# Kernel optimization log

Measured on AMD Instinct MI355X. Metric: run time of the kernel, lower is better.

Reference implementation:

```python
import jax, jax.numpy as jnp
import numpy as np
from jax.scipy.special import logsumexp

PAD_IDX, SOS_IDX, EOS_IDX = 0, 1, 2
NEG = -10000.0


def setup_inputs() -> dict:
    B, T, L = 64, 256, 8
    K, E, H = 128, 256, 512      # num_tags, EMBED_SIZE, HIDDEN_SIZE
    CV, WV = 128, 50000          # char / word vocab
    key = jax.random.key(0)
    ks = jax.random.split(key, 12)
    lengths = jax.random.randint(ks[0], (B,), T // 2, T + 1)
    mask = jnp.arange(T)[None, :] < lengths[:, None]          # [B,T] contiguous prefix
    wx = jnp.where(mask, jax.random.randint(ks[1], (B, T), 3, WV), 0).astype(jnp.int32)
    cx = jax.random.randint(ks[2], (B, T, L), 0, CV).astype(jnp.int32)
    y_body = jnp.where(mask, jax.random.randint(ks[3], (B, T), 3, K), PAD_IDX)
    y = jnp.concatenate([jnp.full((B, 1), SOS_IDX, jnp.int32), y_body.astype(jnp.int32)], 1)  # [B,T+1]
    s = 0.05
    char_emb = s * jax.random.normal(ks[4], (CV, E), jnp.float32)
    word_emb = s * jax.random.normal(ks[5], (WV, E), jnp.float32)
    Wi = s * jax.random.normal(ks[6], (E, 4 * H), jnp.float32)
    Wh = s * jax.random.normal(ks[7], (H, 4 * H), jnp.float32)
    b = jnp.zeros((4 * H,), jnp.float32)
    Wout = s * jax.random.normal(ks[8], (H, K), jnp.float32)
    bout = jnp.zeros((K,), jnp.float32)
    trans = jax.random.normal(ks[9], (K, K), jnp.float32)
    trans = trans.at[SOS_IDX, :].set(NEG)
    trans = trans.at[:, EOS_IDX].set(NEG)
    trans = trans.at[:, PAD_IDX].set(NEG)
    trans = trans.at[PAD_IDX, :].set(NEG)
    trans = trans.at[PAD_IDX, EOS_IDX].set(0.0)
    trans = trans.at[PAD_IDX, PAD_IDX].set(0.0)
    return dict(cx=cx, wx=wx, y=y, char_emb=char_emb, word_emb=word_emb,
                Wi=Wi, Wh=Wh, b=b, Wout=Wout, bout=bout, trans=trans)


def _forward(cx, wx, y, char_emb, word_emb, Wi, Wh, b, Wout, bout, trans):
    B, T = wx.shape
    K = trans.shape[0]
    H = Wh.shape[0]
    mask = (wx > 0)                                            # [B,T] bool
    maskf = mask.astype(jnp.float32)
    # embedding: word lookup + mean-pooled char lookup
    x = word_emb[wx] + char_emb[cx].mean(axis=2)               # [B,T,E]

    # masked LSTM (equivalent to pack_padded for prefix masks)
    def lstm_step(carry, inp):
        h, c = carry
        xt, mt = inp                                            # [B,E], [B,1]
        z = xt @ Wi + h @ Wh + b                                # [B,4H]
        i, f, g, o = jnp.split(z, 4, axis=-1)
        i, f, o = jax.nn.sigmoid(i), jax.nn.sigmoid(f), jax.nn.sigmoid(o)
        c_new = f * c + i * jnp.tanh(g)
        h_new = o * jnp.tanh(c_new)
        h = jnp.where(mt, h_new, h)
        c = jnp.where(mt, c_new, c)
        return (h, c), h

    h0 = jnp.zeros((B, H), x.dtype)
    xs = jnp.swapaxes(x, 0, 1)                                  # [T,B,E]
    ms = jnp.swapaxes(mask, 0, 1)[..., None]                    # [T,B,1]
    _, hs = jax.lax.scan(lstm_step, (h0, h0), (xs, ms))         # [T,B,H]
    hs = jnp.swapaxes(hs, 0, 1)                                 # [B,T,H]
    h = (hs @ Wout + bout) * maskf[..., None]                   # emissions [B,T,K]

    # CRF forward algorithm (log partition Z)
    score0 = jnp.full((B, K), NEG, h.dtype).at[:, SOS_IDX].set(0.0)

    def crf_step(score, inp):
        em, mt = inp                                            # [B,K], [B,1]
        s_t = logsumexp(score[:, None, :] + em[:, :, None] + trans[None, :, :], axis=-1)
        return jnp.where(mt, s_t, score), None

    emT = jnp.swapaxes(h, 0, 1)                                 # [T,B,K]
    scoreZ, _ = jax.lax.scan(crf_step, score0, (emT, ms))
    Z = logsumexp(scoreZ + trans[EOS_IDX], axis=-1)             # [B]

    # gold path score
    y_prev, y_next = y[:, :-1], y[:, 1:]                        # [B,T]
    emit = jnp.take_along_axis(h, y_next[..., None], axis=-1)[..., 0]  # [B,T]
    tr = trans[y_next, y_prev]                                  # [B,T]
    gold = jnp.sum((emit + tr) * maskf, axis=1)                 # [B]
    lengths = mask.sum(axis=1)
    last_tag = y[jnp.arange(B), lengths]                        # y has T+1 cols
    gold = gold + trans[EOS_IDX, last_tag]
    return Z - gold                                             # NLL per sequence [B]


def reference(cx, wx, y, char_emb, word_emb, Wi, Wh, b, Wout, bout, trans):
    return _forward(cx, wx, y, char_emb, word_emb, Wi, Wh, b, Wout, bout, trans)
```

## Files before the change

kernel.cpp:

```cpp
#include <hip/hip_runtime.h>


typedef float f32x4 __attribute__((ext_vector_type(4)));
typedef float f32x16 __attribute__((ext_vector_type(16)));
typedef __bf16 bf16x8 __attribute__((ext_vector_type(8)));
typedef unsigned int u32x4 __attribute__((ext_vector_type(4)));
typedef unsigned int u32x2 __attribute__((ext_vector_type(2)));

#define T_LEN 256
#define BB    64
#define EE    256
#define HH    512
#define KK    128
#define KCAT  768

static __device__ inline unsigned f2bf(float f) {
  union { float f; unsigned u; } v; v.f = f;
  unsigned r = v.u + 0x7FFF + ((v.u >> 16) & 1);
  return r >> 16;
}
static __device__ inline float sigm(float x) { return 1.f / (1.f + __expf(-x)); }
static __device__ inline float tanh_fast(float x) {
  return 1.f - 2.f / (1.f + __expf(2.f * x));
}
static __device__ inline bf16x8 ubf(u32x4 v) {
  union { u32x4 u; bf16x8 b; } c; c.u = v; return c.b;
}

__global__ __launch_bounds__(256) void build_wcat(
    const float* __restrict__ Wi, const float* __restrict__ Wh,
    unsigned short* __restrict__ WcatT) {
  __shared__ float tile[64][65];
  int ct = blockIdx.x & 31, kt = blockIdx.x >> 5;
  int tc = threadIdx.x & 63, tr = threadIdx.x >> 6;
  int c0 = ct * 64, k0 = kt * 64;
#pragma unroll
  for (int i = 0; i < 16; ++i) {
    int r = tr * 16 + i, k = k0 + r;
    float v = (k < EE) ? Wi[(size_t)k * 2048 + c0 + tc]
                       : Wh[(size_t)(k - EE) * 2048 + c0 + tc];
    tile[r][tc] = v;
  }
  __syncthreads();
#pragma unroll
  for (int i = 0; i < 16; ++i) {
    int cL = tr * 16 + i;
    WcatT[(size_t)(c0 + cL) * KCAT + k0 + tc] = (unsigned short)f2bf(tile[tc][cL]);
  }
}

__global__ __launch_bounds__(256) void build_wout(
    const float* __restrict__ Wout, unsigned short* __restrict__ WoutT) {
  __shared__ float tile[64][65];
  int ct = blockIdx.x & 1, kt = blockIdx.x >> 1;
  int tc = threadIdx.x & 63, tr = threadIdx.x >> 6;
  int c0 = ct * 64, k0 = kt * 64;
#pragma unroll
  for (int i = 0; i < 16; ++i) {
    int r = tr * 16 + i;
    tile[r][tc] = Wout[(size_t)(k0 + r) * KK + c0 + tc];
  }
  __syncthreads();
#pragma unroll
  for (int i = 0; i < 16; ++i) {
    int cL = tr * 16 + i;
    WoutT[(size_t)(c0 + cL) * HH + k0 + tc] = (unsigned short)f2bf(tile[tc][cL]);
  }
}

__global__ __launch_bounds__(256) void embed_kernel(
    const int* __restrict__ wx, const int* __restrict__ cx,
    const float* __restrict__ we, const float* __restrict__ ce,
    unsigned short* __restrict__ x) {
  int bid = blockIdx.x;
  int t = bid >> 6, b = bid & 63;
  int e = threadIdx.x;
  int w = wx[b * T_LEN + t];
  float v = we[(size_t)w * EE + e];
  const int* cp = cx + ((size_t)(b * T_LEN + t)) * 8;
  float s = 0.f;
#pragma unroll
  for (int l = 0; l < 8; ++l) s += ce[(size_t)cp[l] * EE + e];
  v += s * 0.125f;
  x[(size_t)bid * EE + e] = (unsigned short)f2bf(v);
}

__global__ void zero_flags(unsigned int* __restrict__ f) {
  int i = threadIdx.x;
  if (i < 320) {
    unsigned z = 0u;
    asm volatile("global_store_dword %0, %1, off sc1"
                 :: "v"(f + i), "v"(z) : "memory");
  }
}

#define SBAR __builtin_amdgcn_sched_barrier(0)
#define WAITV(N) do { asm volatile("s_waitcnt vmcnt(" #N ")" ::: "memory"); SBAR; } while (0)
#define LDN(dst, ptr, OFF) \
  asm volatile("global_load_dwordx4 %0, %1, off offset:" OFF \
               : "=v"(dst) : "v"(ptr) : "memory")

#define ISSUE_X(B, P) do { \
  LDN(B[0],P,"0");   LDN(B[1],P,"32");  LDN(B[2],P,"64");  LDN(B[3],P,"96"); \
  LDN(B[4],P,"128"); LDN(B[5],P,"160"); LDN(B[6],P,"192"); LDN(B[7],P,"224"); \
  LDN(B[8],P,"256"); LDN(B[9],P,"288"); LDN(B[10],P,"320"); LDN(B[11],P,"352"); \
  LDN(B[12],P,"384"); LDN(B[13],P,"416"); LDN(B[14],P,"448"); LDN(B[15],P,"480"); } while (0)
#define ISSUE_H1(B, P) do { \
  LDN(B[0],P,"512"); LDN(B[1],P,"544"); LDN(B[2],P,"576"); LDN(B[3],P,"608"); \
  LDN(B[4],P,"640"); LDN(B[5],P,"672"); LDN(B[6],P,"704"); LDN(B[7],P,"736"); \
  LDN(B[8],P,"768"); LDN(B[9],P,"800"); LDN(B[10],P,"832"); LDN(B[11],P,"864"); \
  LDN(B[12],P,"896"); LDN(B[13],P,"928"); LDN(B[14],P,"960"); LDN(B[15],P,"992"); } while (0)

#define GATES_STORE(T) do { \
    bool mk = ((int)wxv) > 0; \
    _Pragma("unroll") \
    for (int r = 0; r < 4; ++r) { \
      float zi = acc[r], zf = acc[4 + r], zg = acc[8 + r], zo = acc[12 + r]; \
      float cn = sigm(zf) * cst[r] + sigm(zi) * tanh_fast(zg); \
      float hn = sigm(zo) * tanh_fast(cn); \
      if (mk) { cst[r] = cn; hst[r] = hn; } \
    } \
    u32x2 ph; \
    ph[0] = f2bf(hst[0]) | (f2bf(hst[1]) << 16); \
    ph[1] = f2bf(hst[2]) | (f2bf(hst[3]) << 16); \
    asm volatile("global_store_dwordx2 %0, %1, off sc1" \
                 :: "v"(hstore + (size_t)(T) * 65536), "v"(ph) : "memory"); \
  } while (0)

__global__ __launch_bounds__(128, 1) void fused_kernel(
    const unsigned short* __restrict__ x,
    unsigned short* __restrict__ hs,
    const unsigned short* __restrict__ WcatT,
    const unsigned short* __restrict__ WoutT,
    const float* __restrict__ bias,
    const float* __restrict__ bout,
    const float* __restrict__ trans,
    const int* __restrict__ wx,
    const int* __restrict__ y,
    float* __restrict__ em,
    unsigned int* __restrict__ flags,
    unsigned int* __restrict__ emflag,
    float* __restrict__ out) {
  __shared__ float s_tl[KK][129];
  __shared__ float s_El[KK][129];
  __shared__ float s_p[KK];
  __shared__ float s_red[16];

  const int bid = blockIdx.x;
  const int tid = threadIdx.x;
  const int wave = tid >> 6, lane = tid & 63;

  if (bid < 64) {
    const int bhalf = wave;
    const int hi = lane >> 5;
    const int batch = bhalf * 32 + (lane & 31);
    const int u0 = bid * 8;
    const int rr = lane & 31;
    const int wcol = (rr >> 3) * HH + u0 + (rr & 7);

    bf16x8 wreg[48];
#pragma unroll
    for (int kf = 0; kf < 48; ++kf)
      wreg[kf] = *(const bf16x8*)(WcatT + (size_t)wcol * KCAT + kf * 16 + hi * 8);

    float bv[16];
#pragma unroll
    for (int q = 0; q < 4; ++q)
#pragma unroll
      for (int r = 0; r < 4; ++r)
        bv[q * 4 + r] = bias[q * HH + u0 + 4 * hi + r];

    const char* xlane  = (const char*)x  + ((size_t)batch * EE + hi * 8) * 2;
    const char* hread  = (const char*)hs + ((size_t)batch * HH + hi * 8) * 2;
    char*       hstore = (char*)hs + ((size_t)batch * HH + u0 + 4 * hi) * 2;
    const int*  wxp    = wx + batch * T_LEN;

    float cst[4] = {0.f, 0.f, 0.f, 0.f};
    float hst[4] = {0.f, 0.f, 0.f, 0.f};
    u32x4 bufX[16], bufH[16];
    unsigned wxv;
    f32x16 acc;

    ISSUE_X(bufX, xlane);
    asm volatile("global_load_dword %0, %1, off" : "=v"(wxv) : "v"(wxp) : "memory");
    WAITV(0);
#pragma unroll
    for (int i = 0; i < 16; ++i) acc[i] = bv[i];
#pragma unroll
    for (int kf = 0; kf < 16; ++kf)
      acc = __builtin_amdgcn_mfma_f32_32x32x16_bf16(wreg[kf], ubf(bufX[kf]), acc, 0, 0, 0);
    GATES_STORE(0);
    WAITV(0);
    __syncthreads();
    if (tid == 0)
      __hip_atomic_store(flags + bid, 1u, __ATOMIC_RELAXED, __HIP_MEMORY_SCOPE_AGENT);

    for (int t = 1; t < T_LEN; ++t) {
      const char* xt = xlane + (size_t)t * 32768;
      const char* hp = hread + (size_t)(t - 1) * 65536;

      ISSUE_X(bufX, xt);
      asm volatile("global_load_dword %0, %1, off" : "=v"(wxv) : "v"(wxp + t) : "memory");
      {
        unsigned v;
        do {
          asm volatile("global_load_dword %0, %1, off sc1\n\ts_waitcnt vmcnt(0)"
                       : "=v"(v) : "v"(flags + lane) : "memory");
        } while (!__all((int)(v >= (unsigned)t)));
        SBAR;
      }
      ISSUE_X(bufH, hp);
#pragma unroll
      for (int i = 0; i < 16; ++i) acc[i] = bv[i];
#pragma unroll
      for (int kf = 0; kf < 16; ++kf)
        acc = __builtin_amdgcn_mfma_f32_32x32x16_bf16(wreg[kf], ubf(bufX[kf]), acc, 0, 0, 0);
      SBAR;
      ISSUE_H1(bufX, hp);
      WAITV(16);
#pragma unroll
      for (int kf = 0; kf < 16; ++kf)
        acc = __builtin_amdgcn_mfma_f32_32x32x16_bf16(wreg[16 + kf], ubf(bufH[kf]), acc, 0, 0, 0);
      WAITV(0);
#pragma unroll
      for (int kf = 0; kf < 16; ++kf)
        acc = __builtin_amdgcn_mfma_f32_32x32x16_bf16(wreg[32 + kf], ubf(bufX[kf]), acc, 0, 0, 0);
      GATES_STORE(t);
      WAITV(0);
      __syncthreads();
      if (tid == 0)
        __hip_atomic_store(flags + bid, (unsigned)(t + 1),
                           __ATOMIC_RELAXED, __HIP_MEMORY_SCOPE_AGENT);
    }
  } else if (bid < 72) {
    const int et0 = bid - 64;
    const int arow = lane & 15, kg4 = (lane >> 4) * 8;
    for (int i = 0; i < 32; ++i) {
      const int t = et0 + 8 * i;
      {
        unsigned v; int it = 0;
        for (;;) {
          asm volatile("global_load_dword %0, %1, off sc1\n\ts_waitcnt vmcnt(0)"
                       : "=v"(v) : "v"(flags + lane) : "memory");
          if (__all((int)(v >= (unsigned)(t + 1)))) break;
          if (++it >= (1 << 17)) break;
        }
        SBAR;
      }
      const unsigned short* A0 = hs + ((size_t)t * BB + wave * 32 + arow) * HH + kg4;
      f32x4 acc2[2][8];
#pragma unroll
      for (int mt = 0; mt < 2; ++mt)
#pragma unroll
        for (int nt = 0; nt < 8; ++nt) acc2[mt][nt] = (f32x4){0.f, 0.f, 0.f, 0.f};
#pragma unroll
      for (int ks = 0; ks < 16; ++ks) {
        bf16x8 a0 = *(const bf16x8*)(A0 + ks * 32);
        bf16x8 a1 = *(const bf16x8*)(A0 + 16 * HH + ks * 32);
#pragma unroll
        for (int nt = 0; nt < 8; ++nt) {
          bf16x8 bf = *(const bf16x8*)(WoutT + (size_t)(nt * 16 + arow) * HH + kg4 + ks * 32);
          acc2[0][nt] = __builtin_amdgcn_mfma_f32_16x16x32_bf16(a0, bf, acc2[0][nt], 0, 0, 0);
          acc2[1][nt] = __builtin_amdgcn_mfma_f32_16x16x32_bf16(a1, bf, acc2[1][nt], 0, 0, 0);
        }
      }
#pragma unroll
      for (int nt = 0; nt < 8; ++nt) {
        int n = nt * 16 + arow;
        float bo = bout[n];
#pragma unroll
        for (int mt = 0; mt < 2; ++mt)
#pragma unroll
          for (int r = 0; r < 4; ++r) {
            int row = t * BB + wave * 32 + mt * 16 + (lane >> 4) * 4 + r;
            float val = acc2[mt][nt][r] + bo;
            asm volatile("global_store_dword %0, %1, off sc1"
                         :: "v"(em + (size_t)row * KK + n), "v"(val) : "memory");
          }
      }
      WAITV(0);
      __syncthreads();
      if (tid == 0)
        __hip_atomic_store(emflag + t, 1u, __ATOMIC_RELAXED, __HIP_MEMORY_SCOPE_AGENT);
    }
  } else {
    const int b = bid - 72;
    const int k = tid;
    for (int i2 = tid; i2 < KK * KK; i2 += 128) {
      float v = trans[i2];
      s_tl[i2 >> 7][i2 & 127] = v;
      s_El[i2 >> 7][i2 & 127] = __expf(v);
    }
    __syncthreads();
    float sck = (k == 1) ? 0.f : -10000.f;
    float msc = 0.f;

    for (int t = 0; t < T_LEN; ++t) {
      if (wx[b * T_LEN + t] <= 0) continue;
      {
        unsigned v; int it = 0;
        for (;;) {
          asm volatile("global_load_dword %0, %1, off sc1\n\ts_waitcnt vmcnt(0)"
                       : "=v"(v) : "v"(emflag + t) : "memory");
          if (v) break;
          if (++it >= (1 << 17)) break;
        }
        SBAR;
      }
      s_p[k] = __expf(sck - msc);
      __syncthreads();
      float S = 0.f;
#pragma unroll
      for (int j = 0; j < KK; ++j) S += s_El[k][j] * s_p[j];
      float ns = em[((size_t)t * BB + b) * KK + k] + msc + __logf(S);
      sck = ns;
      float m = ns;
#pragma unroll
      for (int off = 32; off; off >>= 1) m = fmaxf(m, __shfl_xor(m, off));
      if (lane == 0) s_red[8 + wave] = m;
      __syncthreads();
      msc = fmaxf(s_red[8], s_red[9]);
    }

    float term = 0.f, cnt = 0.f;
#pragma unroll
    for (int rep = 0; rep < 2; ++rep) {
      int tt = tid + rep * 128;
      int yp = y[b * 257 + tt], yn = y[b * 257 + tt + 1];
      if (wx[b * T_LEN + tt] > 0) {
        term += em[((size_t)tt * BB + b) * KK + yn] + s_tl[yn][yp];
        cnt += 1.f;
      }
    }
#pragma unroll
    for (int off = 32; off; off >>= 1) {
      term += __shfl_xor(term, off);
      cnt += __shfl_xor(cnt, off);
    }
    if (lane == 0) { s_red[wave] = term; s_red[2 + wave] = cnt; }
    __syncthreads();
    float gold = s_red[0] + s_red[1];
    int len = (int)(s_red[2] + s_red[3] + 0.5f);

    float v = sck + s_tl[2][k];
    float mz = v;
#pragma unroll
    for (int off = 32; off; off >>= 1) mz = fmaxf(mz, __shfl_xor(mz, off));
    if (lane == 0) s_red[4 + wave] = mz;
    __syncthreads();
    mz = fmaxf(s_red[4], s_red[5]);
    float e = __expf(v - mz);
#pragma unroll
    for (int off = 32; off; off >>= 1) e += __shfl_xor(e, off);
    if (lane == 0) s_red[6 + wave] = e;
    __syncthreads();
    if (tid == 0) {
      float Z = mz + __logf(s_red[6] + s_red[7]);
      int last_tag = y[b * 257 + len];
      out[b] = Z - (gold + s_tl[2][last_tag]);
    }
  }
}

extern "C" void kernel_launch(void* const* d_in, const int* in_sizes, int n_in,
                              void* d_out, int out_size, void* d_ws, size_t ws_size,
                              hipStream_t stream) {
  const int*   cx    = (const int*)d_in[0];
  const int*   wx    = (const int*)d_in[1];
  const int*   y     = (const int*)d_in[2];
  const float* ce    = (const float*)d_in[3];
  const float* we    = (const float*)d_in[4];
  const float* Wi    = (const float*)d_in[5];
  const float* Wh    = (const float*)d_in[6];
  const float* bias  = (const float*)d_in[7];
  const float* Wout  = (const float*)d_in[8];
  const float* bout  = (const float*)d_in[9];
  const float* trans = (const float*)d_in[10];
  float* out = (float*)d_out;

  char* ws = (char*)d_ws;
  unsigned short* WcatT = (unsigned short*)(ws + 0);
  unsigned short* WoutT = (unsigned short*)(ws + 3145728);
  unsigned short* x     = (unsigned short*)(ws + 3276800);
  unsigned short* hs    = (unsigned short*)(ws + 11665408);
  unsigned int*   flags = (unsigned int*)(ws + 28442624);
  unsigned int*   emflag= (unsigned int*)(ws + 28442880);
  float*          em    = (float*)(ws + 28444672);

  build_wcat<<<384, 256, 0, stream>>>(Wi, Wh, WcatT);
  build_wout<<<16, 256, 0, stream>>>(Wout, WoutT);
  embed_kernel<<<T_LEN * BB, 256, 0, stream>>>(wx, cx, we, ce, x);
  zero_flags<<<1, 320, 0, stream>>>(flags);
  fused_kernel<<<136, 128, 0, stream>>>(x, hs, WcatT, WoutT, bias, bout, trans,
                                        wx, y, em, flags, emflag, out);
}
```

Measured before the change: 1.463 ms.

## Split LSTM into per-batch-group blocks with local flags and fuse emission into CRF

Restructures the persistent LSTM kernel so 128 blocks each handle 8 batch rows and a 32-unit slice using 16x16 MFMAs. Each block now waits only on the 16 producer blocks of its own batch group, through a ring of non-coherent flags with a fallback to coherent polling, instead of on all 64 blocks. The separate emission-projection blocks and the em buffer are removed: each CRF block computes its emissions and gold score from the hidden state with a dot product per timestep. The intent is to cut global synchronisation latency per step and drop the extra em stage. The cost is more CRF work per step and relaxed-visibility flag reads.

```diff
diff --git a/kernel.cpp b/kernel.cpp
--- a/kernel.cpp
+++ b/kernel.cpp
@@ -2,10 +2,8 @@
 
 
 typedef float f32x4 __attribute__((ext_vector_type(4)));
-typedef float f32x16 __attribute__((ext_vector_type(16)));
 typedef __bf16 bf16x8 __attribute__((ext_vector_type(8)));
 typedef unsigned int u32x4 __attribute__((ext_vector_type(4)));
-typedef unsigned int u32x2 __attribute__((ext_vector_type(2)));
 
 #define T_LEN 256
 #define BB    64
@@ -18,6 +16,10 @@
   union { float f; unsigned u; } v; v.f = f;
   unsigned r = v.u + 0x7FFF + ((v.u >> 16) & 1);
   return r >> 16;
+}
+static __device__ inline float bf2f(unsigned short u) {
+  union { unsigned u; float f; } v; v.u = ((unsigned)u) << 16;
+  return v.f;
 }
 static __device__ inline float sigm(float x) { return 1.f / (1.f + __expf(-x)); }
 static __device__ inline float tanh_fast(float x) {
@@ -86,8 +88,8 @@
 }
 
 __global__ void zero_flags(unsigned int* __restrict__ f) {
-  int i = threadIdx.x;
-  if (i < 320) {
+  int i = blockIdx.x * 256 + threadIdx.x;
+  if (i < 128 + 64 * 128) {
     unsigned z = 0u;
     asm volatile("global_store_dword %0, %1, off sc1"
                  :: "v"(f + i), "v"(z) : "memory");
@@ -95,39 +97,21 @@
 }
 
 #define SBAR __builtin_amdgcn_sched_barrier(0)
-#define WAITV(N) do { asm volatile("s_waitcnt vmcnt(" #N ")" ::: "memory"); SBAR; } while (0)
-#define LDN(dst, ptr, OFF) \
+#define WAIT0 do { asm volatile("s_waitcnt vmcnt(0)" ::: "memory"); SBAR; } while (0)
+#define LDN(dst, p, OFF) \
   asm volatile("global_load_dwordx4 %0, %1, off offset:" OFF \
-               : "=v"(dst) : "v"(ptr) : "memory")
-
-#define ISSUE_X(B, P) do { \
-  LDN(B[0],P,"0");   LDN(B[1],P,"32");  LDN(B[2],P,"64");  LDN(B[3],P,"96"); \
-  LDN(B[4],P,"128"); LDN(B[5],P,"160"); LDN(B[6],P,"192"); LDN(B[7],P,"224"); \
-  LDN(B[8],P,"256"); LDN(B[9],P,"288"); LDN(B[10],P,"320"); LDN(B[11],P,"352"); \
-  LDN(B[12],P,"384"); LDN(B[13],P,"416"); LDN(B[14],P,"448"); LDN(B[15],P,"480"); } while (0)
-#define ISSUE_H1(B, P) do { \
-  LDN(B[0],P,"512"); LDN(B[1],P,"544"); LDN(B[2],P,"576"); LDN(B[3],P,"608"); \
-  LDN(B[4],P,"640"); LDN(B[5],P,"672"); LDN(B[6],P,"704"); LDN(B[7],P,"736"); \
-  LDN(B[8],P,"768"); LDN(B[9],P,"800"); LDN(B[10],P,"832"); LDN(B[11],P,"864"); \
-  LDN(B[12],P,"896"); LDN(B[13],P,"928"); LDN(B[14],P,"960"); LDN(B[15],P,"992"); } while (0)
-
-#define GATES_STORE(T) do { \
-    bool mk = ((int)wxv) > 0; \
-    _Pragma("unroll") \
-    for (int r = 0; r < 4; ++r) { \
-      float zi = acc[r], zf = acc[4 + r], zg = acc[8 + r], zo = acc[12 + r]; \
-      float cn = sigm(zf) * cst[r] + sigm(zi) * tanh_fast(zg); \
-      float hn = sigm(zo) * tanh_fast(cn); \
-      if (mk) { cst[r] = cn; hst[r] = hn; } \
-    } \
-    u32x2 ph; \
-    ph[0] = f2bf(hst[0]) | (f2bf(hst[1]) << 16); \
-    ph[1] = f2bf(hst[2]) | (f2bf(hst[3]) << 16); \
-    asm volatile("global_store_dwordx2 %0, %1, off sc1" \
-                 :: "v"(hstore + (size_t)(T) * 65536), "v"(ph) : "memory"); \
-  } while (0)
-
-__global__ __launch_bounds__(128, 1) void fused_kernel(
+               : "=v"(dst) : "v"(p) : "memory")
+
+#define ISSUE_X8(B, P) do { \
+  LDN(B[0],P,"0");   LDN(B[1],P,"64");  LDN(B[2],P,"128"); LDN(B[3],P,"192"); \
+  LDN(B[4],P,"256"); LDN(B[5],P,"320"); LDN(B[6],P,"384"); LDN(B[7],P,"448"); } while (0)
+#define ISSUE_H16(B, P) do { \
+  LDN(B[0],P,"0");   LDN(B[1],P,"64");  LDN(B[2],P,"128"); LDN(B[3],P,"192"); \
+  LDN(B[4],P,"256"); LDN(B[5],P,"320"); LDN(B[6],P,"384"); LDN(B[7],P,"448"); \
+  LDN(B[8],P,"512"); LDN(B[9],P,"576"); LDN(B[10],P,"640"); LDN(B[11],P,"704"); \
+  LDN(B[12],P,"768"); LDN(B[13],P,"832"); LDN(B[14],P,"896"); LDN(B[15],P,"960"); } while (0)
+
+__global__ __launch_bounds__(256, 1) void fused_kernel(
     const unsigned short* __restrict__ x,
     unsigned short* __restrict__ hs,
     const unsigned short* __restrict__ WcatT,
@@ -137,227 +121,217 @@
     const float* __restrict__ trans,
     const int* __restrict__ wx,
     const int* __restrict__ y,
-    float* __restrict__ em,
     unsigned int* __restrict__ flags,
-    unsigned int* __restrict__ emflag,
     float* __restrict__ out) {
-  __shared__ float s_tl[KK][129];
   __shared__ float s_El[KK][129];
+  __shared__ float s_h[HH];
   __shared__ float s_p[KK];
-  __shared__ float s_red[16];
+  __shared__ float s_mv[2 * KK];
+  __shared__ float s_Sp[2 * KK];
+  __shared__ float s_red2[2];
+  __shared__ float s_redg[256];
 
   const int bid = blockIdx.x;
   const int tid = threadIdx.x;
   const int wave = tid >> 6, lane = tid & 63;
-
-  if (bid < 64) {
-    const int bhalf = wave;
-    const int hi = lane >> 5;
-    const int batch = bhalf * 32 + (lane & 31);
-    const int u0 = bid * 8;
-    const int rr = lane & 31;
-    const int wcol = (rr >> 3) * HH + u0 + (rr & 7);
-
-    bf16x8 wreg[48];
-#pragma unroll
-    for (int kf = 0; kf < 48; ++kf)
-      wreg[kf] = *(const bf16x8*)(WcatT + (size_t)wcol * KCAT + kf * 16 + hi * 8);
-
-    float bv[16];
-#pragma unroll
-    for (int q = 0; q < 4; ++q)
-#pragma unroll
-      for (int r = 0; r < 4; ++r)
-        bv[q * 4 + r] = bias[q * HH + u0 + 4 * hi + r];
-
-    const char* xlane  = (const char*)x  + ((size_t)batch * EE + hi * 8) * 2;
-    const char* hread  = (const char*)hs + ((size_t)batch * HH + hi * 8) * 2;
-    char*       hstore = (char*)hs + ((size_t)batch * HH + u0 + 4 * hi) * 2;
-    const int*  wxp    = wx + batch * T_LEN;
-
-    float cst[4] = {0.f, 0.f, 0.f, 0.f};
-    float hst[4] = {0.f, 0.f, 0.f, 0.f};
-    u32x4 bufX[16], bufH[16];
+  unsigned int* flagS = flags;
+  unsigned int* flagE = flags + 128;
+
+  if (bid < 128) {
+    const int g = bid & 7, usl = bid >> 3;
+    const int j = lane & 15, kq = lane >> 4;
+    const int u0 = usl * 32 + wave * 8;
+    const int batch = g * 8 + (j < 8 ? j : 7);
+    const bool jval = (j < 8);
+
+    bf16x8 wreg0[24], wreg1[24];
+#pragma unroll
+    for (int s = 0; s < 24; ++s) {
+      int zc0 = (j & 3) * HH + u0 + 0 + (j >> 2);
+      int zc1 = (j & 3) * HH + u0 + 4 + (j >> 2);
+      wreg0[s] = *(const bf16x8*)(WcatT + (size_t)zc0 * KCAT + s * 32 + kq * 8);
+      wreg1[s] = *(const bf16x8*)(WcatT + (size_t)zc1 * KCAT + s * 32 + kq * 8);
+    }
+    float bv0[4], bv1[4];
+#pragma unroll
+    for (int r = 0; r < 4; ++r) {
+      bv0[r] = bias[r * HH + u0 + 0 + kq];
+      bv1[r] = bias[r * HH + u0 + 4 + kq];
+    }
+
+    const char* xpc = (const char*)x + ((size_t)batch * EE + kq * 8) * 2;
+    const char* hpc = (const char*)hs + ((size_t)batch * HH + kq * 8) * 2;
+    char* hsc = (char*)hs + ((size_t)batch * HH + u0 + kq) * 2;
+    const int* wxp = wx + batch * T_LEN;
+    unsigned int* fSp = flagS + j * 8 + g;
+
+    float cst[2] = {0.f, 0.f}, hst[2] = {0.f, 0.f};
+    u32x4 xf[8], hf[16];
     unsigned wxv;
-    f32x16 acc;
-
-    ISSUE_X(bufX, xlane);
-    asm volatile("global_load_dword %0, %1, off" : "=v"(wxv) : "v"(wxp) : "memory");
-    WAITV(0);
-#pragma unroll
-    for (int i = 0; i < 16; ++i) acc[i] = bv[i];
-#pragma unroll
-    for (int kf = 0; kf < 16; ++kf)
-      acc = __builtin_amdgcn_mfma_f32_32x32x16_bf16(wreg[kf], ubf(bufX[kf]), acc, 0, 0, 0);
-    GATES_STORE(0);
-    WAITV(0);
-    __syncthreads();
-    if (tid == 0)
-      __hip_atomic_store(flags + bid, 1u, __ATOMIC_RELAXED, __HIP_MEMORY_SCOPE_AGENT);
-
-    for (int t = 1; t < T_LEN; ++t) {
-      const char* xt = xlane + (size_t)t * 32768;
-      const char* hp = hread + (size_t)(t - 1) * 65536;
-
-      ISSUE_X(bufX, xt);
+    f32x4 acc0, acc1;
+
+    for (int t = 0; t < T_LEN; ++t) {
+      ISSUE_X8(xf, (xpc + (size_t)t * 32768));
       asm volatile("global_load_dword %0, %1, off" : "=v"(wxv) : "v"(wxp + t) : "memory");
-      {
-        unsigned v;
-        do {
-          asm volatile("global_load_dword %0, %1, off sc1\n\ts_waitcnt vmcnt(0)"
-                       : "=v"(v) : "v"(flags + lane) : "memory");
-        } while (!__all((int)(v >= (unsigned)t)));
-        SBAR;
-      }
-      ISSUE_X(bufH, hp);
-#pragma unroll
-      for (int i = 0; i < 16; ++i) acc[i] = bv[i];
-#pragma unroll
-      for (int kf = 0; kf < 16; ++kf)
-        acc = __builtin_amdgcn_mfma_f32_32x32x16_bf16(wreg[kf], ubf(bufX[kf]), acc, 0, 0, 0);
-      SBAR;
-      ISSUE_H1(bufX, hp);
-      WAITV(16);
-#pragma unroll
-      for (int kf = 0; kf < 16; ++kf)
-        acc = __builtin_amdgcn_mfma_f32_32x32x16_bf16(wreg[16 + kf], ubf(bufH[kf]), acc, 0, 0, 0);
-      WAITV(0);
-#pragma unroll
-      for (int kf = 0; kf < 16; ++kf)
-        acc = __builtin_amdgcn_mfma_f32_32x32x16_bf16(wreg[32 + kf], ubf(bufX[kf]), acc, 0, 0, 0);
-      GATES_STORE(t);
-      WAITV(0);
-      __syncthreads();
-      if (tid == 0)
-        __hip_atomic_store(flags + bid, (unsigned)(t + 1),
-                           __ATOMIC_RELAXED, __HIP_MEMORY_SCOPE_AGENT);
-    }
-  } else if (bid < 72) {
-    const int et0 = bid - 64;
-    const int arow = lane & 15, kg4 = (lane >> 4) * 8;
-    for (int i = 0; i < 32; ++i) {
-      const int t = et0 + 8 * i;
-      {
-        unsigned v; int it = 0;
-        for (;;) {
-          asm volatile("global_load_dword %0, %1, off sc1\n\ts_waitcnt vmcnt(0)"
-                       : "=v"(v) : "v"(flags + lane) : "memory");
-          if (__all((int)(v >= (unsigned)(t + 1)))) break;
-          if (++it >= (1 << 17)) break;
+      if (t > 0) {
+        unsigned int* fEp = flagE + (t & 63) * 128 + j * 8 + g;
+        bool ok = false;
+        for (int it = 0; it < 64; ++it) {
+          unsigned v;
+          asm volatile("global_load_dword %0, %1, off\n\ts_waitcnt vmcnt(0)"
+                       : "=v"(v) : "v"(fEp) : "memory");
+          if (__all((int)(v >= (unsigned)t))) { ok = true; break; }
+        }
+        if (!ok) {
+          unsigned v;
+          do {
+            asm volatile("global_load_dword %0, %1, off sc1\n\ts_waitcnt vmcnt(0)"
+                         : "=v"(v) : "v"(fSp) : "memory");
+          } while (!__all((int)(v >= (unsigned)t)));
         }
         SBAR;
-      }
-      const unsigned short* A0 = hs + ((size_t)t * BB + wave * 32 + arow) * HH + kg4;
-      f32x4 acc2[2][8];
-#pragma unroll
-      for (int mt = 0; mt < 2; ++mt)
-#pragma unroll
-        for (int nt = 0; nt < 8; ++nt) acc2[mt][nt] = (f32x4){0.f, 0.f, 0.f, 0.f};
-#pragma unroll
-      for (int ks = 0; ks < 16; ++ks) {
-        bf16x8 a0 = *(const bf16x8*)(A0 + ks * 32);
-        bf16x8 a1 = *(const bf16x8*)(A0 + 16 * HH + ks * 32);
-#pragma unroll
-        for (int nt = 0; nt < 8; ++nt) {
-          bf16x8 bf = *(const bf16x8*)(WoutT + (size_t)(nt * 16 + arow) * HH + kg4 + ks * 32);
-          acc2[0][nt] = __builtin_amdgcn_mfma_f32_16x16x32_bf16(a0, bf, acc2[0][nt], 0, 0, 0);
-          acc2[1][nt] = __builtin_amdgcn_mfma_f32_16x16x32_bf16(a1, bf, acc2[1][nt], 0, 0, 0);
+        ISSUE_H16(hf, (hpc + (size_t)(t - 1) * 65536));
+      } else {
+        WAIT0;
+      }
+#pragma unroll
+      for (int r = 0; r < 4; ++r) { acc0[r] = bv0[r]; acc1[r] = bv1[r]; }
+#pragma unroll
+      for (int f = 0; f < 8; ++f) {
+        bf16x8 d = ubf(xf[f]);
+        acc0 = __builtin_amdgcn_mfma_f32_16x16x32_bf16(wreg0[f], d, acc0, 0, 0, 0);
+        acc1 = __builtin_amdgcn_mfma_f32_16x16x32_bf16(wreg1[f], d, acc1, 0, 0, 0);
+      }
+      if (t > 0) {
+        WAIT0;
+#pragma unroll
+        for (int f = 0; f < 16; ++f) {
+          bf16x8 d = ubf(hf[f]);
+          acc0 = __builtin_amdgcn_mfma_f32_16x16x32_bf16(wreg0[8 + f], d, acc0, 0, 0, 0);
+          acc1 = __builtin_amdgcn_mfma_f32_16x16x32_bf16(wreg1[8 + f], d, acc1, 0, 0, 0);
         }
       }
-#pragma unroll
-      for (int nt = 0; nt < 8; ++nt) {
-        int n = nt * 16 + arow;
-        float bo = bout[n];
-#pragma unroll
-        for (int mt = 0; mt < 2; ++mt)
-#pragma unroll
-          for (int r = 0; r < 4; ++r) {
-            int row = t * BB + wave * 32 + mt * 16 + (lane >> 4) * 4 + r;
-            float val = acc2[mt][nt][r] + bo;
-            asm volatile("global_store_dword %0, %1, off sc1"
-                         :: "v"(em + (size_t)row * KK + n), "v"(val) : "memory");
-          }
-      }
-      WAITV(0);
-      __syncthreads();
-      if (tid == 0)
-        __hip_atomic_store(emflag + t, 1u, __ATOMIC_RELAXED, __HIP_MEMORY_SCOPE_AGENT);
+      bool mk = ((int)wxv) > 0;
+      {
+        float cn = sigm(acc0[1]) * cst[0] + sigm(acc0[0]) * tanh_fast(acc0[2]);
+        float hn = sigm(acc0[3]) * tanh_fast(cn);
+        if (mk) { cst[0] = cn; hst[0] = hn; }
+        float cn1 = sigm(acc1[1]) * cst[1] + sigm(acc1[0]) * tanh_fast(acc1[2]);
+        float hn1 = sigm(acc1[3]) * tanh_fast(cn1);
+        if (mk) { cst[1] = cn1; hst[1] = hn1; }
+      }
+      if (jval) {
+        unsigned v0 = f2bf(hst[0]), v1 = f2bf(hst[1]);
+        asm volatile("global_store_short %0, %1, off sc1"
+                     :: "v"(hsc + (size_t)t * 65536), "v"(v0) : "memory");
+        asm volatile("global_store_short %0, %1, off offset:8 sc1"
+                     :: "v"(hsc + (size_t)t * 65536), "v"(v1) : "memory");
+      }
+      WAIT0;
+      __syncthreads();
+      if (tid == 0) {
+        unsigned nv = (unsigned)(t + 1);
+        asm volatile("global_store_dword %0, %1, off sc1"
+                     :: "v"(flagS + bid), "v"(nv) : "memory");
+        asm volatile("global_store_dword %0, %1, off"
+                     :: "v"(flagE + ((t + 1) & 63) * 128 + bid), "v"(nv) : "memory");
+      }
     }
   } else {
-    const int b = bid - 72;
-    const int k = tid;
-    for (int i2 = tid; i2 < KK * KK; i2 += 128) {
-      float v = trans[i2];
-      s_tl[i2 >> 7][i2 & 127] = v;
-      s_El[i2 >> 7][i2 & 127] = __expf(v);
-    }
-    __syncthreads();
+    const int b = bid - 128;
+    const int gq = b >> 3;
+    const int k = tid & 127, half = tid >> 7;
+    for (int i = tid; i < KK * KK; i += 256)
+      s_El[i >> 7][i & 127] = __expf(trans[i]);
+    __syncthreads();
+
     float sck = (k == 1) ? 0.f : -10000.f;
-    float msc = 0.f;
+    float msc = 0.f, gold = 0.f;
+    int len = 0;
+    unsigned int* fSp = flagS + (lane & 15) * 8 + gq;
 
     for (int t = 0; t < T_LEN; ++t) {
       if (wx[b * T_LEN + t] <= 0) continue;
       {
         unsigned v; int it = 0;
-        for (;;) {
+        do {
           asm volatile("global_load_dword %0, %1, off sc1\n\ts_waitcnt vmcnt(0)"
-                       : "=v"(v) : "v"(emflag + t) : "memory");
-          if (v) break;
-          if (++it >= (1 << 17)) break;
+                       : "=v"(v) : "v"(fSp) : "memory");
+          if (__all((int)(v >= (unsigned)(t + 1)))) break;
+        } while (++it < (1 << 20));
+        SBAR;
+      }
+      {
+        unsigned hv = *(const unsigned*)(hs + ((size_t)t * BB + b) * HH + tid * 2);
+        s_h[tid * 2]     = bf2f((unsigned short)(hv & 0xffff));
+        s_h[tid * 2 + 1] = bf2f((unsigned short)(hv >> 16));
+      }
+      __syncthreads();
+      float e = 0.f;
+      const char* wp = (const char*)WoutT + ((size_t)k * HH + half * 256) * 2;
+#pragma unroll 8
+      for (int f = 0; f < 32; ++f) {
+        u32x4 wv = *(const u32x4*)(wp + f * 16);
+        const float* hb = s_h + half * 256 + f * 8;
+#pragma unroll
+        for (int d = 0; d < 4; ++d) {
+          e += hb[d * 2]     * bf2f((unsigned short)(wv[d] & 0xffff));
+          e += hb[d * 2 + 1] * bf2f((unsigned short)(wv[d] >> 16));
         }
-        SBAR;
-      }
-      s_p[k] = __expf(sck - msc);
+      }
+      s_mv[half * KK + k] = e;
+      __syncthreads();
+      float em_k = s_mv[k] + s_mv[KK + k] + bout[k];
+      if (tid < KK) s_p[tid] = __expf(sck - msc);
       __syncthreads();
       float S = 0.f;
 #pragma unroll
-      for (int j = 0; j < KK; ++j) S += s_El[k][j] * s_p[j];
-      float ns = em[((size_t)t * BB + b) * KK + k] + msc + __logf(S);
+      for (int jj = 0; jj < 64; ++jj) S += s_El[k][half * 64 + jj] * s_p[half * 64 + jj];
+      s_Sp[half * KK + k] = S;
+      __syncthreads();
+      float ns = em_k + msc + __logf(s_Sp[k] + s_Sp[KK + k]);
+      int yn = y[b * 257 + t + 1];
+      if (half == 0 && k == yn) gold += em_k + trans[yn * KK + y[b * 257 + t]];
+      len++;
       sck = ns;
-      float m = ns;
-#pragma unroll
-      for (int off = 32; off; off >>= 1) m = fmaxf(m, __shfl_xor(m, off));
-      if (lane == 0) s_red[8 + wave] = m;
-      __syncthreads();
-      msc = fmaxf(s_red[8], s_red[9]);
-    }
-
-    float term = 0.f, cnt = 0.f;
-#pragma unroll
-    for (int rep = 0; rep < 2; ++rep) {
-      int tt = tid + rep * 128;
-      int yp = y[b * 257 + tt], yn = y[b * 257 + tt + 1];
-      if (wx[b * T_LEN + tt] > 0) {
-        term += em[((size_t)tt * BB + b) * KK + yn] + s_tl[yn][yp];
-        cnt += 1.f;
-      }
-    }
-#pragma unroll
-    for (int off = 32; off; off >>= 1) {
-      term += __shfl_xor(term, off);
-      cnt += __shfl_xor(cnt, off);
-    }
-    if (lane == 0) { s_red[wave] = term; s_red[2 + wave] = cnt; }
-    __syncthreads();
-    float gold = s_red[0] + s_red[1];
-    int len = (int)(s_red[2] + s_red[3] + 0.5f);
-
-    float v = sck + s_tl[2][k];
-    float mz = v;
-#pragma unroll
-    for (int off = 32; off; off >>= 1) mz = fmaxf(mz, __shfl_xor(mz, off));
-    if (lane == 0) s_red[4 + wave] = mz;
-    __syncthreads();
-    mz = fmaxf(s_red[4], s_red[5]);
-    float e = __expf(v - mz);
-#pragma unroll
-    for (int off = 32; off; off >>= 1) e += __shfl_xor(e, off);
-    if (lane == 0) s_red[6 + wave] = e;
-    __syncthreads();
+      if (half == 0) {
+        float m = ns;
+#pragma unroll
+        for (int off = 32; off; off >>= 1) m = fmaxf(m, __shfl_xor(m, off));
+        if (lane == 0) s_red2[wave] = m;
+      }
+      __syncthreads();
+      msc = fmaxf(s_red2[0], s_red2[1]);
+    }
+
+    s_redg[tid] = gold;
+    __syncthreads();
+    for (int s2 = 128; s2 > 0; s2 >>= 1) {
+      if (tid < s2) s_redg[tid] += s_redg[tid + s2];
+      __syncthreads();
+    }
+    gold = s_redg[0];
+    __syncthreads();
+
+    float v = sck + trans[2 * KK + k];
+    if (half == 0) s_redg[k] = v; else s_redg[128 + k] = -3.0e38f;
+    __syncthreads();
+    for (int s2 = 64; s2 > 0; s2 >>= 1) {
+      if (tid < s2) s_redg[tid] = fmaxf(s_redg[tid], s_redg[tid + s2]);
+      __syncthreads();
+    }
+    float mz = s_redg[0];
+    __syncthreads();
+    s_redg[tid] = (half == 0) ? __expf(v - mz) : 0.f;
+    __syncthreads();
+    for (int s2 = 128; s2 > 0; s2 >>= 1) {
+      if (tid < s2) s_redg[tid] += s_redg[tid + s2];
+      __syncthreads();
+    }
     if (tid == 0) {
-      float Z = mz + __logf(s_red[6] + s_red[7]);
+      float Z = mz + __logf(s_redg[0]);
       int last_tag = y[b * 257 + len];
-      out[b] = Z - (gold + s_tl[2][last_tag]);
+      out[b] = Z - (gold + trans[2 * KK + last_tag]);
     }
   }
 }
@@ -384,13 +358,11 @@
   unsigned short* x     = (unsigned short*)(ws + 3276800);
   unsigned short* hs    = (unsigned short*)(ws + 11665408);
   unsigned int*   flags = (unsigned int*)(ws + 28442624);
-  unsigned int*   emflag= (unsigned int*)(ws + 28442880);
-  float*          em    = (float*)(ws + 28444672);
 
   build_wcat<<<384, 256, 0, stream>>>(Wi, Wh, WcatT);
   build_wout<<<16, 256, 0, stream>>>(Wout, WoutT);
   embed_kernel<<<T_LEN * BB, 256, 0, stream>>>(wx, cx, we, ce, x);
-  zero_flags<<<1, 320, 0, stream>>>(flags);
-  fused_kernel<<<136, 128, 0, stream>>>(x, hs, WcatT, WoutT, bias, bout, trans,
-                                        wx, y, em, flags, emflag, out);
-}
+  zero_flags<<<33, 256, 0, stream>>>(flags);
+  fused_kernel<<<192, 256, 0, stream>>>(x, hs, WcatT, WoutT, bias, bout, trans,
+                                        wx, y, flags, out);
+}
```

After: 1.894 ms. 29.4% more time.
